# Optimization experiments

Measured on AMD Instinct MI355X. Metric: run time of the kernel, lower is better.

Reference implementation:

```python
import jax, jax.numpy as jnp
import numpy as np

H = 16  # num_heads

def setup_inputs() -> dict:
    key = jax.random.key(0)
    ks = jax.random.split(key, 5)
    d = 1024
    s = 0.02
    return {
        'x': jax.random.normal(ks[0], (2, 2048, d), jnp.float32),
        'Wq': jax.random.normal(ks[1], (d, d), jnp.float32) * s,
        'bq': jnp.zeros((d,), jnp.float32),
        'Wk': jax.random.normal(ks[2], (d, d), jnp.float32) * s,
        'bk': jnp.zeros((d,), jnp.float32),
        'Wv': jax.random.normal(ks[3], (d, d), jnp.float32) * s,
        'bv': jnp.zeros((d,), jnp.float32),
        'Wo': jax.random.normal(ks[4], (d, d), jnp.float32) * s,
        'bo': jnp.zeros((d,), jnp.float32),
        'ln_scale': jnp.ones((d,), jnp.float32),
        'ln_bias': jnp.zeros((d,), jnp.float32),
    }

def _layernorm(x, scale, bias, eps=1e-6):
    mu = jnp.mean(x, axis=-1, keepdims=True)
    var = jnp.var(x, axis=-1, keepdims=True)
    return (x - mu) * jax.lax.rsqrt(var + eps) * scale + bias

def reference(x, Wq, bq, Wk, bk, Wv, bv, Wo, bo, ln_scale, ln_bias):
    b, n, d = x.shape
    hd = d // H
    scale = hd ** -0.5
    residual = x
    xn = _layernorm(x, ln_scale, ln_bias)
    # QKV projections, split heads: [b, n, d] -> [b, H, n, hd]
    def split(y):
        return y.reshape(b, n, H, hd).transpose(0, 2, 1, 3)
    q = split(xn @ Wq + bq)
    k = split(xn @ Wk + bk)
    v = split(xn @ Wv + bv)
    attn = jnp.einsum('bhid,bhjd->bhij', q, k) * scale
    attn = jax.nn.softmax(attn, axis=-1)
    out = jnp.einsum('bhij,bhjd->bhid', attn, v)
    out = out.transpose(0, 2, 1, 3).reshape(b, n, d)
    out = out @ Wo + bo
    return out + residual
```

## Files before the change

kernel.cpp:

```cpp
#include <hip/hip_runtime.h>

typedef __bf16 bf16;
typedef __bf16 bf16x8 __attribute__((ext_vector_type(8)));
typedef float f32x4 __attribute__((ext_vector_type(4)));

#define D_MODEL 1024
#define SEQ 2048
#define NH 16
#define HD 64

#define GLD16(gp, lp) __builtin_amdgcn_global_load_lds( \
    (const __attribute__((address_space(1))) void*)(gp), \
    (__attribute__((address_space(3))) void*)(lp), 16, 0, 0)

__device__ __forceinline__ int sigp(int r) {
    return (r & 0x23) | ((r & 0x0C) << 1) | ((r & 0x10) >> 2);
}

__global__ __launch_bounds__(256) void ln_kernel(const float* __restrict__ x,
        const float* __restrict__ g, const float* __restrict__ bta,
        bf16* __restrict__ xnb) {
    int tok = blockIdx.x;
    const float* xr = x + (size_t)tok * D_MODEL;
    float v[4];
    float s = 0.f, ss = 0.f;
#pragma unroll
    for (int j = 0; j < 4; ++j) {
        int idx = threadIdx.x + j * 256;
        float t = xr[idx];
        v[j] = t; s += t; ss += t * t;
    }
#pragma unroll
    for (int m = 32; m; m >>= 1) { s += __shfl_xor(s, m, 64); ss += __shfl_xor(ss, m, 64); }
    __shared__ float red_s[4], red_ss[4];
    int w = threadIdx.x >> 6;
    if ((threadIdx.x & 63) == 0) { red_s[w] = s; red_ss[w] = ss; }
    __syncthreads();
    s  = red_s[0] + red_s[1] + red_s[2] + red_s[3];
    ss = red_ss[0] + red_ss[1] + red_ss[2] + red_ss[3];
    float mu  = s * (1.f / D_MODEL);
    float var = ss * (1.f / D_MODEL) - mu * mu;
    float rstd = rsqrtf(var + 1e-6f);
    bf16* orow = xnb + (size_t)tok * D_MODEL;
#pragma unroll
    for (int j = 0; j < 4; ++j) {
        int idx = threadIdx.x + j * 256;
        float xn = (v[j] - mu) * rstd * g[idx] + bta[idx];
        orow[idx] = (bf16)xn;
    }
}

__global__ __launch_bounds__(256) void transpose_kernel(const float* __restrict__ W0,
        const float* __restrict__ W1, const float* __restrict__ W2,
        const float* __restrict__ W3, bf16* __restrict__ wt) {
    __shared__ float tile[32][33];
    int mat = blockIdx.z;
    const float* W = mat == 0 ? W0 : mat == 1 ? W1 : mat == 2 ? W2 : W3;
    bf16* dst = wt + (size_t)mat * D_MODEL * D_MODEL;
    int k0 = blockIdx.x * 32, n0 = blockIdx.y * 32;
    int tx = threadIdx.x & 31, ty0 = threadIdx.x >> 5;
#pragma unroll
    for (int r = 0; r < 4; ++r) {
        int ty = ty0 + r * 8;
        tile[ty][tx] = W[(size_t)(k0 + ty) * D_MODEL + n0 + tx];
    }
    __syncthreads();
#pragma unroll
    for (int r = 0; r < 4; ++r) {
        int ty = ty0 + r * 8;
        dst[(size_t)(n0 + ty) * D_MODEL + k0 + tx] = (bf16)tile[tx][ty];
    }
}

__global__ __launch_bounds__(256) void qkv_gemm(const bf16* __restrict__ A,
        const bf16* __restrict__ Bt, const float* __restrict__ bq,
        const float* __restrict__ bk, const float* __restrict__ bv,
        bf16* __restrict__ qo, bf16* __restrict__ ko, bf16* __restrict__ vto) {
    __shared__ __align__(16) bf16 As[128 * 32];
    __shared__ __align__(16) bf16 Bs[128 * 32];
    int m0 = blockIdx.x * 128, n0 = blockIdx.y * 128;
    int tid = threadIdx.x;
    int w = tid >> 6, l = tid & 63, lm = l & 15, lq = l >> 4;
    int wm = (w >> 1) * 64, wn = (w & 1) * 64;
    f32x4 acc[4][4] = {};
    const bf16* ag = A  + (size_t)(m0 + w * 32 + (l >> 2)) * D_MODEL + (l & 3) * 8;
    const bf16* bg = Bt + (size_t)(n0 + w * 32 + (l >> 2)) * D_MODEL + (l & 3) * 8;
    bf16* asd = &As[(w * 32) * 32];
    bf16* bsd = &Bs[(w * 32) * 32];
    for (int k0 = 0; k0 < D_MODEL; k0 += 32) {
        GLD16(ag,                asd);
        GLD16(ag + 16 * D_MODEL, asd + 16 * 32);
        GLD16(bg,                bsd);
        GLD16(bg + 16 * D_MODEL, bsd + 16 * 32);
        ag += 32; bg += 32;
        __syncthreads();
        bf16x8 af[4], bf_[4];
#pragma unroll
        for (int f = 0; f < 4; ++f) af[f]  = *(const bf16x8*)&As[(wm + f * 16 + lm) * 32 + lq * 8];
#pragma unroll
        for (int f = 0; f < 4; ++f) bf_[f] = *(const bf16x8*)&Bs[(wn + f * 16 + lm) * 32 + lq * 8];
#pragma unroll
        for (int fm = 0; fm < 4; ++fm)
#pragma unroll
            for (int fn = 0; fn < 4; ++fn)
                acc[fm][fn] = __builtin_amdgcn_mfma_f32_16x16x32_bf16(af[fm], bf_[fn], acc[fm][fn], 0, 0, 0);
        __syncthreads();
    }
#pragma unroll
    for (int fn = 0; fn < 4; ++fn) {
        int n_g = n0 + wn + fn * 16 + lm;
        int mat = n_g >> 10, within = n_g & 1023;
        int h = within >> 6, hdp = within & 63;
        float bias = mat == 0 ? bq[within] : mat == 1 ? bk[within] : bv[within];
#pragma unroll
        for (int fm = 0; fm < 4; ++fm) {
#pragma unroll
            for (int r = 0; r < 4; ++r) {
                int m_g = m0 + wm + fm * 16 + lq * 4 + r;
                int b_ = m_g >> 11, i = m_g & 2047;
                int bh = b_ * NH + h;
                float val = acc[fm][fn][r] + bias;
                if (mat == 0)      qo [((size_t)bh * SEQ + i) * HD + hdp] = (bf16)(val * 0.180336888f);
                else if (mat == 1) ko [((size_t)bh * SEQ + i) * HD + hdp] = (bf16)val;
                else               vto[((size_t)bh * HD + hdp) * SEQ + i] = (bf16)val;
            }
        }
    }
}

__global__ __launch_bounds__(256) void attn_kernel(const bf16* __restrict__ q,
        const bf16* __restrict__ k, const bf16* __restrict__ vt,
        bf16* __restrict__ aout) {
    __shared__ __align__(16) bf16 Qs[128][72];
    __shared__ __align__(16) bf16 Ks[64 * 64];
    __shared__ __align__(16) bf16 Vs[64 * 64];
    int i0 = blockIdx.x * 128;
    int bh = blockIdx.y;
    int tid = threadIdx.x;
    int w = tid >> 6, l = tid & 63, lm = l & 15, lq = l >> 4;
    const bf16* qb = q + (size_t)bh * SEQ * HD;
    const bf16* kb = k + (size_t)bh * SEQ * HD;
    const bf16* vb = vt + (size_t)bh * HD * SEQ;

    {
        int tr = tid >> 1, half = tid & 1;
#pragma unroll
        for (int c = 0; c < 4; ++c) {
            int col = half * 32 + c * 8;
            *(uint4*)&Qs[tr][col] = *(const uint4*)(qb + (size_t)(i0 + tr) * HD + col);
        }
    }
    int row0 = w * 16 + (l >> 3);
    int g = l & 7;
    const bf16* ks0 = kb + (size_t)sigp(row0) * HD     + (size_t)((g ^ (row0 & 7)) * 8);
    const bf16* ks1 = kb + (size_t)sigp(row0 + 8) * HD + (size_t)((g ^ ((row0 + 8) & 7)) * 8);
    const bf16* vs0 = vb + (size_t)row0 * SEQ       + (size_t)((g ^ (row0 & 7)) * 8);
    const bf16* vs1 = vb + (size_t)(row0 + 8) * SEQ + (size_t)((g ^ ((row0 + 8) & 7)) * 8);
    bf16* kd0 = &Ks[(w * 16) * 64];
    bf16* kd1 = &Ks[(w * 16 + 8) * 64];
    bf16* vd0 = &Vs[(w * 16) * 64];
    bf16* vd1 = &Vs[(w * 16 + 8) * 64];

    __syncthreads();
    bf16x8 qf[2][2];
#pragma unroll
    for (int mf = 0; mf < 2; ++mf)
#pragma unroll
        for (int kc = 0; kc < 2; ++kc)
            qf[mf][kc] = *(const bf16x8*)&Qs[w * 32 + mf * 16 + lm][kc * 32 + lq * 8];

    f32x4 o[2][4] = {};
    float l_acc[2] = {0.f, 0.f};

    for (int j0 = 0; j0 < SEQ; j0 += 64) {
        GLD16(ks0, kd0); GLD16(ks1, kd1);
        GLD16(vs0, vd0); GLD16(vs1, vd1);
        ks0 += 64 * HD; ks1 += 64 * HD; vs0 += 64; vs1 += 64;
        __syncthreads();
        f32x4 s[2][4] = {};
#pragma unroll
        for (int kc = 0; kc < 2; ++kc) {
#pragma unroll
            for (int nt = 0; nt < 4; ++nt) {
                int r = nt * 16 + lm;
                int gl = (kc * 4 + lq) ^ (lm & 7);
                bf16x8 kf = *(const bf16x8*)&Ks[r * 64 + gl * 8];
                s[0][nt] = __builtin_amdgcn_mfma_f32_16x16x32_bf16(kf, qf[0][kc], s[0][nt], 0, 0, 0);
                s[1][nt] = __builtin_amdgcn_mfma_f32_16x16x32_bf16(kf, qf[1][kc], s[1][nt], 0, 0, 0);
            }
        }
#pragma unroll
        for (int mf = 0; mf < 2; ++mf) {
            float psum = 0.f;
#pragma unroll
            for (int nt = 0; nt < 4; ++nt)
#pragma unroll
                for (int r = 0; r < 4; ++r) {
                    float p = exp2f(s[mf][nt][r]);
                    s[mf][nt][r] = p; psum += p;
                }
            l_acc[mf] += psum;
        }
#pragma unroll
        for (int kc = 0; kc < 2; ++kc) {
            bf16x8 pf[2];
#pragma unroll
            for (int mf = 0; mf < 2; ++mf)
#pragma unroll
                for (int jj = 0; jj < 8; ++jj)
                    pf[mf][jj] = (bf16)s[mf][2 * kc + (jj >> 2)][jj & 3];
#pragma unroll
            for (int nt = 0; nt < 4; ++nt) {
                int p = nt * 16 + lm;
                int gl = (kc * 4 + lq) ^ (lm & 7);
                bf16x8 vf = *(const bf16x8*)&Vs[p * 64 + gl * 8];
                o[0][nt] = __builtin_amdgcn_mfma_f32_16x16x32_bf16(pf[0], vf, o[0][nt], 0, 0, 0);
                o[1][nt] = __builtin_amdgcn_mfma_f32_16x16x32_bf16(pf[1], vf, o[1][nt], 0, 0, 0);
            }
        }
        __syncthreads();
    }
    int b_ = bh >> 4, h = bh & 15;
#pragma unroll
    for (int mf = 0; mf < 2; ++mf) {
        l_acc[mf] += __shfl_xor(l_acc[mf], 16, 64);
        l_acc[mf] += __shfl_xor(l_acc[mf], 32, 64);
        float linv[4];
#pragma unroll
        for (int r = 0; r < 4; ++r)
            linv[r] = 1.f / __shfl(l_acc[mf], lq * 4 + r, 64);
#pragma unroll
        for (int nt = 0; nt < 4; ++nt) {
#pragma unroll
            for (int r = 0; r < 4; ++r) {
                int i = i0 + w * 32 + mf * 16 + lq * 4 + r;
                int tok = b_ * SEQ + i;
                aout[(size_t)tok * D_MODEL + h * HD + nt * 16 + lm] = (bf16)(o[mf][nt][r] * linv[r]);
            }
        }
    }
}

__global__ __launch_bounds__(256) void out_gemm(const bf16* __restrict__ A,
        const bf16* __restrict__ Bt, const float* __restrict__ bo,
        const float* __restrict__ resid, float* __restrict__ out) {
    __shared__ __align__(16) bf16 As[128 * 32];
    __shared__ __align__(16) bf16 Bs[128 * 32];
    int m0 = blockIdx.x * 128, n0 = blockIdx.y * 128;
    int tid = threadIdx.x;
    int w = tid >> 6, l = tid & 63, lm = l & 15, lq = l >> 4;
    int wm = (w >> 1) * 64, wn = (w & 1) * 64;
    f32x4 acc[4][4] = {};
    const bf16* ag = A  + (size_t)(m0 + w * 32 + (l >> 2)) * D_MODEL + (l & 3) * 8;
    const bf16* bg = Bt + (size_t)(n0 + w * 32 + (l >> 2)) * D_MODEL + (l & 3) * 8;
    bf16* asd = &As[(w * 32) * 32];
    bf16* bsd = &Bs[(w * 32) * 32];
    for (int k0 = 0; k0 < D_MODEL; k0 += 32) {
        GLD16(ag,                asd);
        GLD16(ag + 16 * D_MODEL, asd + 16 * 32);
        GLD16(bg,                bsd);
        GLD16(bg + 16 * D_MODEL, bsd + 16 * 32);
        ag += 32; bg += 32;
        __syncthreads();
        bf16x8 af[4], bf_[4];
#pragma unroll
        for (int f = 0; f < 4; ++f) af[f]  = *(const bf16x8*)&As[(wm + f * 16 + lm) * 32 + lq * 8];
#pragma unroll
        for (int f = 0; f < 4; ++f) bf_[f] = *(const bf16x8*)&Bs[(wn + f * 16 + lm) * 32 + lq * 8];
#pragma unroll
        for (int fm = 0; fm < 4; ++fm)
#pragma unroll
            for (int fn = 0; fn < 4; ++fn)
                acc[fm][fn] = __builtin_amdgcn_mfma_f32_16x16x32_bf16(af[fm], bf_[fn], acc[fm][fn], 0, 0, 0);
        __syncthreads();
    }
#pragma unroll
    for (int fn = 0; fn < 4; ++fn) {
        int n_g = n0 + wn + fn * 16 + lm;
        float bias = bo[n_g];
#pragma unroll
        for (int fm = 0; fm < 4; ++fm) {
#pragma unroll
            for (int r = 0; r < 4; ++r) {
                int m_g = m0 + wm + fm * 16 + lq * 4 + r;
                size_t idx = (size_t)m_g * D_MODEL + n_g;
                out[idx] = acc[fm][fn][r] + bias + resid[idx];
            }
        }
    }
}

extern "C" void kernel_launch(void* const* d_in, const int* in_sizes, int n_in,
                              void* d_out, int out_size, void* d_ws, size_t ws_size,
                              hipStream_t stream) {
    const float* x  = (const float*)d_in[0];
    const float* Wq = (const float*)d_in[1];
    const float* bq = (const float*)d_in[2];
    const float* Wk = (const float*)d_in[3];
    const float* bk = (const float*)d_in[4];
    const float* Wv = (const float*)d_in[5];
    const float* bv = (const float*)d_in[6];
    const float* Wo = (const float*)d_in[7];
    const float* bo = (const float*)d_in[8];
    const float* g  = (const float*)d_in[9];
    const float* bt = (const float*)d_in[10];
    (void)in_sizes; (void)n_in; (void)out_size; (void)ws_size;

    char* ws = (char*)d_ws;
    const size_t M8 = (size_t)8 << 20;
    bf16* xnb = (bf16*)(ws);
    bf16* wt  = (bf16*)(ws + M8);
    bf16* qb  = (bf16*)(ws + 2 * M8);
    bf16* kb  = (bf16*)(ws + 3 * M8);
    bf16* vtb = (bf16*)(ws + 4 * M8);
    bf16* ao  = xnb;
    float* out = (float*)d_out;

    ln_kernel<<<4096, 256, 0, stream>>>(x, g, bt, xnb);
    transpose_kernel<<<dim3(32, 32, 4), 256, 0, stream>>>(Wq, Wk, Wv, Wo, wt);
    qkv_gemm<<<dim3(32, 24), 256, 0, stream>>>(xnb, wt, bq, bk, bv, qb, kb, vtb);
    attn_kernel<<<dim3(16, 32), 256, 0, stream>>>(qb, kb, vtb, ao);
    out_gemm<<<dim3(32, 8), 256, 0, stream>>>(ao, wt + (size_t)3 * D_MODEL * D_MODEL, bo, x, out);
}
```

Baseline: 222.9 us.

## Double-buffer K/V tiles in attention via register prefetch, drop trailing barrier

New measurement: 217.4 us. -2.5%, faster.

```diff
diff --git a/kernel.cpp b/kernel.cpp
--- a/kernel.cpp
+++ b/kernel.cpp
@@ -131,9 +131,8 @@
 __global__ __launch_bounds__(256) void attn_kernel(const bf16* __restrict__ q,
         const bf16* __restrict__ k, const bf16* __restrict__ vt,
         bf16* __restrict__ aout) {
-    __shared__ __align__(16) bf16 Qs[128][72];
-    __shared__ __align__(16) bf16 Ks[64 * 64];
-    __shared__ __align__(16) bf16 Vs[64 * 64];
+    __shared__ __align__(16) bf16 Ks[2][64 * 64];
+    __shared__ __align__(16) bf16 Vs[2][64 * 64];
     int i0 = blockIdx.x * 128;
     int bh = blockIdx.y;
     int tid = threadIdx.x;
@@ -142,40 +141,38 @@
     const bf16* kb = k + (size_t)bh * SEQ * HD;
     const bf16* vb = vt + (size_t)bh * HD * SEQ;
 
-    {
-        int tr = tid >> 1, half = tid & 1;
-#pragma unroll
-        for (int c = 0; c < 4; ++c) {
-            int col = half * 32 + c * 8;
-            *(uint4*)&Qs[tr][col] = *(const uint4*)(qb + (size_t)(i0 + tr) * HD + col);
-        }
-    }
-    int row0 = w * 16 + (l >> 3);
+    bf16x8 qf[2][2];
+#pragma unroll
+    for (int mf = 0; mf < 2; ++mf)
+#pragma unroll
+        for (int kc = 0; kc < 2; ++kc)
+            qf[mf][kc] = *(const bf16x8*)(qb + (size_t)(i0 + w * 32 + mf * 16 + lm) * HD + kc * 32 + lq * 8);
+
+    int r0 = w * 16 + (l >> 3), r1 = r0 + 8;
     int g = l & 7;
-    const bf16* ks0 = kb + (size_t)sigp(row0) * HD     + (size_t)((g ^ (row0 & 7)) * 8);
-    const bf16* ks1 = kb + (size_t)sigp(row0 + 8) * HD + (size_t)((g ^ ((row0 + 8) & 7)) * 8);
-    const bf16* vs0 = vb + (size_t)row0 * SEQ       + (size_t)((g ^ (row0 & 7)) * 8);
-    const bf16* vs1 = vb + (size_t)(row0 + 8) * SEQ + (size_t)((g ^ ((row0 + 8) & 7)) * 8);
-    bf16* kd0 = &Ks[(w * 16) * 64];
-    bf16* kd1 = &Ks[(w * 16 + 8) * 64];
-    bf16* vd0 = &Vs[(w * 16) * 64];
-    bf16* vd1 = &Vs[(w * 16 + 8) * 64];
-
-    __syncthreads();
-    bf16x8 qf[2][2];
-#pragma unroll
-    for (int mf = 0; mf < 2; ++mf)
-#pragma unroll
-        for (int kc = 0; kc < 2; ++kc)
-            qf[mf][kc] = *(const bf16x8*)&Qs[w * 32 + mf * 16 + lm][kc * 32 + lq * 8];
+    const bf16* kp0 = kb + (size_t)sigp(r0) * HD + g * 8;
+    const bf16* kp1 = kb + (size_t)sigp(r1) * HD + g * 8;
+    const bf16* vp0 = vb + (size_t)r0 * SEQ + g * 8;
+    const bf16* vp1 = vb + (size_t)r1 * SEQ + g * 8;
+    int d0 = r0 * 64 + ((g ^ (r0 & 7)) * 8);
+    int d1 = r1 * 64 + ((g ^ (r1 & 7)) * 8);
+
+    uint4 kr0 = *(const uint4*)kp0, kr1 = *(const uint4*)kp1;
+    uint4 vr0 = *(const uint4*)vp0, vr1 = *(const uint4*)vp1;
+    kp0 += 64 * HD; kp1 += 64 * HD; vp0 += 64; vp1 += 64;
 
     f32x4 o[2][4] = {};
     float l_acc[2] = {0.f, 0.f};
 
     for (int j0 = 0; j0 < SEQ; j0 += 64) {
-        GLD16(ks0, kd0); GLD16(ks1, kd1);
-        GLD16(vs0, vd0); GLD16(vs1, vd1);
-        ks0 += 64 * HD; ks1 += 64 * HD; vs0 += 64; vs1 += 64;
+        int b = (j0 >> 6) & 1;
+        *(uint4*)&Ks[b][d0] = kr0; *(uint4*)&Ks[b][d1] = kr1;
+        *(uint4*)&Vs[b][d0] = vr0; *(uint4*)&Vs[b][d1] = vr1;
+        if (j0 + 64 < SEQ) {
+            kr0 = *(const uint4*)kp0; kr1 = *(const uint4*)kp1;
+            vr0 = *(const uint4*)vp0; vr1 = *(const uint4*)vp1;
+            kp0 += 64 * HD; kp1 += 64 * HD; vp0 += 64; vp1 += 64;
+        }
         __syncthreads();
         f32x4 s[2][4] = {};
 #pragma unroll
@@ -184,7 +181,7 @@
             for (int nt = 0; nt < 4; ++nt) {
                 int r = nt * 16 + lm;
                 int gl = (kc * 4 + lq) ^ (lm & 7);
-                bf16x8 kf = *(const bf16x8*)&Ks[r * 64 + gl * 8];
+                bf16x8 kf = *(const bf16x8*)&Ks[b][r * 64 + gl * 8];
                 s[0][nt] = __builtin_amdgcn_mfma_f32_16x16x32_bf16(kf, qf[0][kc], s[0][nt], 0, 0, 0);
                 s[1][nt] = __builtin_amdgcn_mfma_f32_16x16x32_bf16(kf, qf[1][kc], s[1][nt], 0, 0, 0);
             }
@@ -213,12 +210,11 @@
             for (int nt = 0; nt < 4; ++nt) {
                 int p = nt * 16 + lm;
                 int gl = (kc * 4 + lq) ^ (lm & 7);
-                bf16x8 vf = *(const bf16x8*)&Vs[p * 64 + gl * 8];
+                bf16x8 vf = *(const bf16x8*)&Vs[b][p * 64 + gl * 8];
                 o[0][nt] = __builtin_amdgcn_mfma_f32_16x16x32_bf16(pf[0], vf, o[0][nt], 0, 0, 0);
                 o[1][nt] = __builtin_amdgcn_mfma_f32_16x16x32_bf16(pf[1], vf, o[1][nt], 0, 0, 0);
             }
         }
-        __syncthreads();
     }
     int b_ = bh >> 4, h = bh & 15;
 #pragma unroll
```
